# Optimization experiments

Measured on AMD Instinct MI355X. Metric: run time of the kernel, lower is better.

The kernel has to match this reference:

```python
import jax, jax.numpy as jnp
import numpy as np

EMBED_DIM = 512
NUM_HEADS = 8
HEAD_DIM = EMBED_DIM // NUM_HEADS


def setup_inputs() -> dict:
    key = jax.random.key(0)
    ks = jax.random.split(key, 9)
    d = EMBED_DIM
    s = 1.0 / np.sqrt(d)
    inp = {
        "x": jax.random.normal(ks[0], (2, 4096, d), dtype=jnp.float32),
        # torch nn.Linear weights are [out, in]; we store them the same way
        "Wq": jax.random.uniform(ks[1], (d, d), jnp.float32, -s, s),
        "bq": jax.random.uniform(ks[2], (d,), jnp.float32, -s, s),
        "Wk": jax.random.uniform(ks[3], (d, d), jnp.float32, -s, s),
        "bk": jax.random.uniform(ks[4], (d,), jnp.float32, -s, s),
        "Wv": jax.random.uniform(ks[5], (d, d), jnp.float32, -s, s),
        "bv": jax.random.uniform(ks[6], (d,), jnp.float32, -s, s),
        "Wo": jax.random.uniform(ks[7], (d, d), jnp.float32, -s, s),
        "bo": jax.random.uniform(ks[8], (d,), jnp.float32, -s, s),
    }
    return inp


def reference(x, Wq, bq, Wk, bk, Wv, bv, Wo, bo):
    B, S, D = x.shape
    H, Hd = NUM_HEADS, HEAD_DIM

    def proj(W, b):  # torch Linear: x @ W.T + b
        y = jnp.einsum("bsd,ed->bse", x, W) + b
        return y.reshape(B, S, H, Hd).transpose(0, 2, 1, 3)  # [B,H,S,Hd]

    Q = proj(Wq, bq)
    K = proj(Wk, bk)
    V = proj(Wv, bv)

    scale = 1.0 / jnp.sqrt(jnp.float32(Hd))
    scores = jnp.einsum("bhqd,bhkd->bhqk", Q, K) * scale  # [B,H,S,S]
    attn = jax.nn.softmax(scores, axis=-1)
    out = jnp.einsum("bhqk,bhkd->bhqd", attn, V)  # [B,H,S,Hd]
    out = out.transpose(0, 2, 1, 3).reshape(B, S, D)
    return jnp.einsum("bsd,ed->bse", out, Wo) + bo
```

## Files before the change

### kernel.cpp

```cpp
#include <hip/hip_runtime.h>


typedef unsigned short ushortT;
typedef __attribute__((ext_vector_type(8))) short short8;
typedef __attribute__((ext_vector_type(4))) float f32x4;
typedef __attribute__((ext_vector_type(16))) float f32x16;
typedef __attribute__((ext_vector_type(4))) unsigned int uint4v;
typedef __attribute__((ext_vector_type(2))) unsigned int uint2v;

__device__ __forceinline__ ushortT f2bf(float f) {
    unsigned int u = __builtin_bit_cast(unsigned int, f);
    u += 0x7FFFu + ((u >> 16) & 1u);
    return (ushortT)(u >> 16);
}

__device__ __forceinline__ unsigned int cvtpk(float lo, float hi) {
    unsigned int d;
    asm("v_cvt_pk_bf16_f32 %0, %1, %2" : "=v"(d) : "v"(lo), "v"(hi));
    return d;
}

__device__ __forceinline__ uint4v pk8(f32x4 a0, f32x4 a1) {
    uint4v r = { cvtpk(a0[0], a0[1]), cvtpk(a0[2], a0[3]),
                 cvtpk(a1[0], a1[1]), cvtpk(a1[2], a1[3]) };
    return r;
}

__device__ __forceinline__ uint4v ldpk8(const float* p) {
    f32x4 a0 = *(const f32x4*)p;
    f32x4 a1 = *(const f32x4*)(p + 4);
    return pk8(a0, a1);
}

__device__ __forceinline__ void plswap(unsigned int &a, unsigned int &b) {
    uint2v r = __builtin_amdgcn_permlane32_swap(a, b, false, false);
    a = r[0]; b = r[1];
}

#define GLDB 72
#define ALDK 72

__global__ __launch_bounds__(512, 4) void proj_qkv(
    const float* __restrict__ x,
    const float* __restrict__ Wq, const float* __restrict__ bq,
    const float* __restrict__ Wk, const float* __restrict__ bk,
    const float* __restrict__ Wv, const float* __restrict__ bv,
    ushortT* __restrict__ Qw, ushortT* __restrict__ Kw,
    ushortT* __restrict__ Vtw, float qscale)
{
    __shared__ __align__(16) ushortT As[128 * GLDB];
    __shared__ __align__(16) ushortT Bs[128 * GLDB];
    const int t = threadIdx.x;
    const int w = t >> 6, lane = t & 63;
    const int quad = lane >> 4, l15 = lane & 15;
    const int z = blockIdx.z;
    const int bx = blockIdx.x, by = blockIdx.y;
    const int wm = (w >> 1) * 32, wn = (w & 1) * 64;

    const float* W    = (z == 0) ? Wq : (z == 1) ? Wk : Wv;
    const float* bias = (z == 0) ? bq : (z == 1) ? bk : bv;
    const float* Asrc = (z < 2) ? x : W;
    const float* Bsrc = (z < 2) ? W : x;
    const int arow0 = (z < 2) ? bx * 128 : by * 128;
    const int brow0 = (z < 2) ? by * 128 : bx * 128;

    const int sr0 = t >> 3, sc0 = (t & 7) * 8;

    uint4v pka[2], pkb[2];
    pka[0] = ldpk8(Asrc + (size_t)(arow0 + sr0) * 512 + sc0);
    pka[1] = ldpk8(Asrc + (size_t)(arow0 + sr0 + 64) * 512 + sc0);
    pkb[0] = ldpk8(Bsrc + (size_t)(brow0 + sr0) * 512 + sc0);
    pkb[1] = ldpk8(Bsrc + (size_t)(brow0 + sr0 + 64) * 512 + sc0);

    f32x4 acc[2][4] = {};

    for (int k0 = 0; k0 < 512; k0 += 64) {
        *(uint4v*)(As + sr0 * GLDB + sc0) = pka[0];
        *(uint4v*)(As + (sr0 + 64) * GLDB + sc0) = pka[1];
        *(uint4v*)(Bs + sr0 * GLDB + sc0) = pkb[0];
        *(uint4v*)(Bs + (sr0 + 64) * GLDB + sc0) = pkb[1];
        __syncthreads();

        if (k0 < 448) {
            const int kn = k0 + 64;
            pka[0] = ldpk8(Asrc + (size_t)(arow0 + sr0) * 512 + kn + sc0);
            pka[1] = ldpk8(Asrc + (size_t)(arow0 + sr0 + 64) * 512 + kn + sc0);
            pkb[0] = ldpk8(Bsrc + (size_t)(brow0 + sr0) * 512 + kn + sc0);
            pkb[1] = ldpk8(Bsrc + (size_t)(brow0 + sr0 + 64) * 512 + kn + sc0);
        }

#pragma unroll
        for (int kk = 0; kk < 2; kk++) {
            short8 af[2], bfr[4];
#pragma unroll
            for (int i = 0; i < 2; i++)
                af[i] = *(const short8*)(As + (wm + i * 16 + l15) * GLDB + kk * 32 + quad * 8);
#pragma unroll
            for (int i = 0; i < 4; i++)
                bfr[i] = *(const short8*)(Bs + (wn + i * 16 + l15) * GLDB + kk * 32 + quad * 8);
#pragma unroll
            for (int mi = 0; mi < 2; mi++)
#pragma unroll
                for (int ni = 0; ni < 4; ni++)
                    acc[mi][ni] = __builtin_amdgcn_mfma_f32_16x16x32_bf16(
                        af[mi], bfr[ni], acc[mi][ni], 0, 0, 0);
        }
        __syncthreads();
    }

    if (z < 2) {
        ushortT* Y = (z == 0) ? Qw : Kw;
        const float sc = (z == 0) ? qscale : 1.0f;
#pragma unroll
        for (int ni = 0; ni < 4; ni++) {
            int col = brow0 + wn + ni * 16 + l15;
            float bv_ = bias[col];
#pragma unroll
            for (int mi = 0; mi < 2; mi++)
#pragma unroll
                for (int r = 0; r < 4; r++) {
                    int row = arow0 + wm + mi * 16 + quad * 4 + r;
                    Y[(size_t)row * 512 + col] = f2bf((acc[mi][ni][r] + bv_) * sc);
                }
        }
    } else {
        const int bidx = brow0 >> 12;
        const int s0 = brow0 & 4095;
#pragma unroll
        for (int mi = 0; mi < 2; mi++)
#pragma unroll
            for (int r = 0; r < 4; r++) {
                int ch = arow0 + wm + mi * 16 + quad * 4 + r;
                float bv_ = bias[ch];
#pragma unroll
                for (int ni = 0; ni < 4; ni++) {
                    int s = s0 + wn + ni * 16 + l15;
                    Vtw[(size_t)bidx * 2097152 + (size_t)ch * 4096 + s] =
                        f2bf(acc[mi][ni][r] + bv_);
                }
            }
    }
}

__global__ __launch_bounds__(512, 4) void gemm_out(
    const ushortT* __restrict__ X, const float* __restrict__ W,
    const float* __restrict__ bias, float* __restrict__ Y)
{
    __shared__ __align__(16) ushortT As[128 * GLDB];
    __shared__ __align__(16) ushortT Bs[128 * GLDB];
    const int t = threadIdx.x;
    const int w = t >> 6, lane = t & 63;
    const int quad = lane >> 4, l15 = lane & 15;
    const int bm = blockIdx.x * 128, bn = blockIdx.y * 128;
    const int wm = (w >> 1) * 32, wn = (w & 1) * 64;

    const int sr0 = t >> 3, sc0 = (t & 7) * 8;

    uint4v pa[2], pkb[2];
    pa[0] = *(const uint4v*)(X + (size_t)(bm + sr0) * 512 + sc0);
    pa[1] = *(const uint4v*)(X + (size_t)(bm + sr0 + 64) * 512 + sc0);
    pkb[0] = ldpk8(W + (size_t)(bn + sr0) * 512 + sc0);
    pkb[1] = ldpk8(W + (size_t)(bn + sr0 + 64) * 512 + sc0);

    f32x4 acc[2][4] = {};

    for (int k0 = 0; k0 < 512; k0 += 64) {
        *(uint4v*)(As + sr0 * GLDB + sc0) = pa[0];
        *(uint4v*)(As + (sr0 + 64) * GLDB + sc0) = pa[1];
        *(uint4v*)(Bs + sr0 * GLDB + sc0) = pkb[0];
        *(uint4v*)(Bs + (sr0 + 64) * GLDB + sc0) = pkb[1];
        __syncthreads();

        if (k0 < 448) {
            const int kn = k0 + 64;
            pa[0] = *(const uint4v*)(X + (size_t)(bm + sr0) * 512 + kn + sc0);
            pa[1] = *(const uint4v*)(X + (size_t)(bm + sr0 + 64) * 512 + kn + sc0);
            pkb[0] = ldpk8(W + (size_t)(bn + sr0) * 512 + kn + sc0);
            pkb[1] = ldpk8(W + (size_t)(bn + sr0 + 64) * 512 + kn + sc0);
        }

#pragma unroll
        for (int kk = 0; kk < 2; kk++) {
            short8 af[2], bfr[4];
#pragma unroll
            for (int i = 0; i < 2; i++)
                af[i] = *(const short8*)(As + (wm + i * 16 + l15) * GLDB + kk * 32 + quad * 8);
#pragma unroll
            for (int i = 0; i < 4; i++)
                bfr[i] = *(const short8*)(Bs + (wn + i * 16 + l15) * GLDB + kk * 32 + quad * 8);
#pragma unroll
            for (int mi = 0; mi < 2; mi++)
#pragma unroll
                for (int ni = 0; ni < 4; ni++)
                    acc[mi][ni] = __builtin_amdgcn_mfma_f32_16x16x32_bf16(
                        af[mi], bfr[ni], acc[mi][ni], 0, 0, 0);
        }
        __syncthreads();
    }

#pragma unroll
    for (int ni = 0; ni < 4; ni++) {
        int col = bn + wn + ni * 16 + l15;
        float bv = bias[col];
#pragma unroll
        for (int mi = 0; mi < 2; mi++)
#pragma unroll
            for (int r = 0; r < 4; r++) {
                int row = bm + wm + mi * 16 + quad * 4 + r;
                Y[(size_t)row * 512 + col] = acc[mi][ni][r] + bv;
            }
    }
}

__device__ __forceinline__ void softmax_pack(const f32x16 &sacc, float &lp,
                                             uint4v &B0, uint4v &B1)
{
    float p[16];
#pragma unroll
    for (int r = 0; r < 16; r++) {
        p[r] = __builtin_amdgcn_exp2f(sacc[r]);
        lp += p[r];
    }
    unsigned int c00 = cvtpk(p[0],  p[1]),  c01 = cvtpk(p[2],  p[3]);
    unsigned int c10 = cvtpk(p[4],  p[5]),  c11 = cvtpk(p[6],  p[7]);
    unsigned int c20 = cvtpk(p[8],  p[9]),  c21 = cvtpk(p[10], p[11]);
    unsigned int c30 = cvtpk(p[12], p[13]), c31 = cvtpk(p[14], p[15]);
    plswap(c00, c10);
    plswap(c01, c11);
    plswap(c20, c30);
    plswap(c21, c31);
    B0 = uint4v{ c00, c01, c10, c11 };
    B1 = uint4v{ c20, c21, c30, c31 };
}

__global__ __launch_bounds__(512, 2) void attn(
    const ushortT* Q, const ushortT* __restrict__ K,
    const ushortT* __restrict__ Vt, ushortT* O)
{
    __shared__ __align__(16) ushortT SM[2][2][2][64 * ALDK];

    const int t = threadIdx.x;
    const int w = t >> 6, lane = t & 63;
    const int half = w >> 2, qw = w & 3;
    const int l31 = lane & 31, hh = lane >> 5;
    const int qt = blockIdx.x, bh = blockIdx.y;
    const int b = bh >> 3, h = bh & 7;
    const size_t qbase = (size_t)b * 4096 + qt * 256 + qw * 64;

    short8 qf[2][4];
#pragma unroll
    for (int qg = 0; qg < 2; qg++) {
        const ushortT* qp = Q + (qbase + qg * 32 + l31) * 512 + h * 64 + hh * 8;
#pragma unroll
        for (int dk = 0; dk < 4; dk++)
            qf[qg][dk] = *(const short8*)(qp + dk * 16);
    }

    f32x16 oacc[2][2] = {};
    float lpart[2] = {};

    const int kofs = half * 2048;
    const ushortT* Kbase = K + ((size_t)b * 4096 + kofs) * 512 + h * 64;
    const ushortT* Vbase = Vt + (size_t)b * 2097152 + (size_t)h * 64 * 4096 + kofs;

    const int th = t & 255;
    const int srow = th >> 3, scol = (th & 7) * 8;
    uint4v kg[2], vg[2];

#pragma unroll
    for (int i = 0; i < 2; i++) {
        kg[i] = *(const uint4v*)(Kbase + (size_t)(srow + 32 * i) * 512 + scol);
        vg[i] = *(const uint4v*)(Vbase + (size_t)(srow + 32 * i) * 4096 + scol);
    }
#pragma unroll
    for (int i = 0; i < 2; i++) {
        *(uint4v*)(SM[0][half][0] + (srow + 32 * i) * ALDK + scol) = kg[i];
        *(uint4v*)(SM[1][half][0] + (srow + 32 * i) * ALDK + scol) = vg[i];
    }
    __syncthreads();

    for (int kt = 0; kt < 32; kt++) {
        const int cur = kt & 1;

        if (kt < 31) {
            const int kb = (kt + 1) * 64;
#pragma unroll
            for (int i = 0; i < 2; i++) {
                kg[i] = *(const uint4v*)(Kbase + (size_t)(kb + srow + 32 * i) * 512 + scol);
                vg[i] = *(const uint4v*)(Vbase + (size_t)(srow + 32 * i) * 4096 + kb + scol);
            }
        }

        const ushortT* Kt  = SM[0][half][cur];
        const ushortT* Vtl = SM[1][half][cur];

#pragma unroll
        for (int st = 0; st < 2; st++) {
            short8 kf[4];
#pragma unroll
            for (int dk = 0; dk < 4; dk++)
                kf[dk] = *(const short8*)(Kt + (st * 32 + l31) * ALDK + dk * 16 + hh * 8);
            f32x16 s0 = {}, s1 = {};
#pragma unroll
            for (int dk = 0; dk < 4; dk++) {
                s0 = __builtin_amdgcn_mfma_f32_32x32x16_bf16(kf[dk], qf[0][dk], s0, 0, 0, 0);
                s1 = __builtin_amdgcn_mfma_f32_32x32x16_bf16(kf[dk], qf[1][dk], s1, 0, 0, 0);
            }

            uint4v B00, B01, B10, B11;
            softmax_pack(s0, lpart[0], B00, B01);
            softmax_pack(s1, lpart[1], B10, B11);
            short8 p00 = __builtin_bit_cast(short8, B00);
            short8 p01 = __builtin_bit_cast(short8, B01);
            short8 p10 = __builtin_bit_cast(short8, B10);
            short8 p11 = __builtin_bit_cast(short8, B11);

#pragma unroll
            for (int dt = 0; dt < 2; dt++) {
                short8 vf0 = *(const short8*)(Vtl + (dt * 32 + l31) * ALDK + st * 32 + hh * 8);
                short8 vf1 = *(const short8*)(Vtl + (dt * 32 + l31) * ALDK + st * 32 + 16 + hh * 8);
                oacc[0][dt] = __builtin_amdgcn_mfma_f32_32x32x16_bf16(vf0, p00, oacc[0][dt], 0, 0, 0);
                oacc[0][dt] = __builtin_amdgcn_mfma_f32_32x32x16_bf16(vf1, p01, oacc[0][dt], 0, 0, 0);
                oacc[1][dt] = __builtin_amdgcn_mfma_f32_32x32x16_bf16(vf0, p10, oacc[1][dt], 0, 0, 0);
                oacc[1][dt] = __builtin_amdgcn_mfma_f32_32x32x16_bf16(vf1, p11, oacc[1][dt], 0, 0, 0);
            }
        }

        if (kt < 31) {
            const int nb = cur ^ 1;
#pragma unroll
            for (int i = 0; i < 2; i++) {
                *(uint4v*)(SM[0][half][nb] + (srow + 32 * i) * ALDK + scol) = kg[i];
                *(uint4v*)(SM[1][half][nb] + (srow + 32 * i) * ALDK + scol) = vg[i];
            }
        }
        __syncthreads();
    }

    float* scratch = (float*)&SM[0][0][0][0];
    float* prow = scratch + (size_t)(qw * 64 + lane) * 68;

    if (half == 1) {
#pragma unroll
        for (int qg = 0; qg < 2; qg++)
#pragma unroll
            for (int dt = 0; dt < 2; dt++)
#pragma unroll
                for (int m = 0; m < 4; m++) {
                    f32x4 v4 = { oacc[qg][dt][4 * m + 0], oacc[qg][dt][4 * m + 1],
                                 oacc[qg][dt][4 * m + 2], oacc[qg][dt][4 * m + 3] };
                    *(f32x4*)(prow + qg * 32 + dt * 16 + m * 4) = v4;
                }
        prow[64] = lpart[0];
        prow[65] = lpart[1];
    }
    __syncthreads();

    if (half == 0) {
#pragma unroll
        for (int qg = 0; qg < 2; qg++) {
            float sum = lpart[qg] + prow[64 + qg];
            float l = sum + __shfl_xor(sum, 32);
            float rl = 1.0f / l;

            ushortT* orow = O + (qbase + qg * 32 + l31) * 512 + h * 64 + hh * 4;
#pragma unroll
            for (int dt = 0; dt < 2; dt++)
#pragma unroll
                for (int m = 0; m < 4; m++) {
                    f32x4 v4 = *(const f32x4*)(prow + qg * 32 + dt * 16 + m * 4);
                    unsigned int u0 = cvtpk((oacc[qg][dt][4 * m + 0] + v4[0]) * rl,
                                            (oacc[qg][dt][4 * m + 1] + v4[1]) * rl);
                    unsigned int u1 = cvtpk((oacc[qg][dt][4 * m + 2] + v4[2]) * rl,
                                            (oacc[qg][dt][4 * m + 3] + v4[3]) * rl);
                    uint2v st2 = { u0, u1 };
                    *(uint2v*)(orow + dt * 32 + m * 8) = st2;
                }
        }
    }
}

extern "C" void kernel_launch(void* const* d_in, const int* in_sizes, int n_in,
                              void* d_out, int out_size, void* d_ws, size_t ws_size,
                              hipStream_t stream)
{
    const float* x  = (const float*)d_in[0];
    const float* Wq = (const float*)d_in[1];
    const float* bq = (const float*)d_in[2];
    const float* Wk = (const float*)d_in[3];
    const float* bk = (const float*)d_in[4];
    const float* Wv = (const float*)d_in[5];
    const float* bv = (const float*)d_in[6];
    const float* Wo = (const float*)d_in[7];
    const float* bo = (const float*)d_in[8];

    ushortT* ws  = (ushortT*)d_ws;
    ushortT* Qw  = ws;
    ushortT* Kw  = ws + 4194304;
    ushortT* Vtw = ws + 2 * 4194304;

    const float qscale = 0.125f * 1.44269504089f;

    proj_qkv<<<dim3(64, 4, 3), 512, 0, stream>>>(
        x, Wq, bq, Wk, bk, Wv, bv, Qw, Kw, Vtw, qscale);
    attn<<<dim3(16, 16), 512, 0, stream>>>(Qw, Kw, Vtw, Qw);
    gemm_out<<<dim3(64, 4), 512, 0, stream>>>(Qw, Wo, bo, (float*)d_out);
}
```

Baseline: 196.6 us.

## Fuse Q/K/V projections into one block sharing the x tile

The QKV projection kernel now computes all three projections in one block. Each x tile is loaded and converted to bf16 once and reused against three weight tiles, where before three separate z-slices each reloaded it. The V output is now computed as x·Wv^T instead of Wv·x^T, with a transposed store using packed 2-element bf16 writes. The grid shrinks to a third and each block holds three accumulator sets and three B tiles in LDS. That raises register and LDS pressure, so the launch bound drops to 2 blocks per CU.

```diff
diff --git a/kernel.cpp b/kernel.cpp
--- a/kernel.cpp
+++ b/kernel.cpp
@@ -40,7 +40,7 @@
 #define GLDB 72
 #define ALDK 72
 
-__global__ __launch_bounds__(512, 4) void proj_qkv(
+__global__ __launch_bounds__(512, 2) void proj_qkv(
     const float* __restrict__ x,
     const float* __restrict__ Wq, const float* __restrict__ bq,
     const float* __restrict__ Wk, const float* __restrict__ bk,
@@ -49,67 +49,77 @@
     ushortT* __restrict__ Vtw, float qscale)
 {
     __shared__ __align__(16) ushortT As[128 * GLDB];
-    __shared__ __align__(16) ushortT Bs[128 * GLDB];
+    __shared__ __align__(16) ushortT Bs[3][128 * GLDB];
     const int t = threadIdx.x;
     const int w = t >> 6, lane = t & 63;
     const int quad = lane >> 4, l15 = lane & 15;
-    const int z = blockIdx.z;
-    const int bx = blockIdx.x, by = blockIdx.y;
+    const int arow0 = blockIdx.x * 128;
+    const int brow0 = blockIdx.y * 128;
     const int wm = (w >> 1) * 32, wn = (w & 1) * 64;
 
-    const float* W    = (z == 0) ? Wq : (z == 1) ? Wk : Wv;
-    const float* bias = (z == 0) ? bq : (z == 1) ? bk : bv;
-    const float* Asrc = (z < 2) ? x : W;
-    const float* Bsrc = (z < 2) ? W : x;
-    const int arow0 = (z < 2) ? bx * 128 : by * 128;
-    const int brow0 = (z < 2) ? by * 128 : bx * 128;
+    const float* Wsrc[3] = { Wq, Wk, Wv };
 
     const int sr0 = t >> 3, sc0 = (t & 7) * 8;
 
-    uint4v pka[2], pkb[2];
-    pka[0] = ldpk8(Asrc + (size_t)(arow0 + sr0) * 512 + sc0);
-    pka[1] = ldpk8(Asrc + (size_t)(arow0 + sr0 + 64) * 512 + sc0);
-    pkb[0] = ldpk8(Bsrc + (size_t)(brow0 + sr0) * 512 + sc0);
-    pkb[1] = ldpk8(Bsrc + (size_t)(brow0 + sr0 + 64) * 512 + sc0);
-
-    f32x4 acc[2][4] = {};
+    uint4v pka[2], pkb[3][2];
+    pka[0] = ldpk8(x + (size_t)(arow0 + sr0) * 512 + sc0);
+    pka[1] = ldpk8(x + (size_t)(arow0 + sr0 + 64) * 512 + sc0);
+#pragma unroll
+    for (int z = 0; z < 3; z++) {
+        pkb[z][0] = ldpk8(Wsrc[z] + (size_t)(brow0 + sr0) * 512 + sc0);
+        pkb[z][1] = ldpk8(Wsrc[z] + (size_t)(brow0 + sr0 + 64) * 512 + sc0);
+    }
+
+    f32x4 acc[3][2][4] = {};
 
     for (int k0 = 0; k0 < 512; k0 += 64) {
         *(uint4v*)(As + sr0 * GLDB + sc0) = pka[0];
         *(uint4v*)(As + (sr0 + 64) * GLDB + sc0) = pka[1];
-        *(uint4v*)(Bs + sr0 * GLDB + sc0) = pkb[0];
-        *(uint4v*)(Bs + (sr0 + 64) * GLDB + sc0) = pkb[1];
+#pragma unroll
+        for (int z = 0; z < 3; z++) {
+            *(uint4v*)(Bs[z] + sr0 * GLDB + sc0) = pkb[z][0];
+            *(uint4v*)(Bs[z] + (sr0 + 64) * GLDB + sc0) = pkb[z][1];
+        }
         __syncthreads();
 
         if (k0 < 448) {
             const int kn = k0 + 64;
-            pka[0] = ldpk8(Asrc + (size_t)(arow0 + sr0) * 512 + kn + sc0);
-            pka[1] = ldpk8(Asrc + (size_t)(arow0 + sr0 + 64) * 512 + kn + sc0);
-            pkb[0] = ldpk8(Bsrc + (size_t)(brow0 + sr0) * 512 + kn + sc0);
-            pkb[1] = ldpk8(Bsrc + (size_t)(brow0 + sr0 + 64) * 512 + kn + sc0);
+            pka[0] = ldpk8(x + (size_t)(arow0 + sr0) * 512 + kn + sc0);
+            pka[1] = ldpk8(x + (size_t)(arow0 + sr0 + 64) * 512 + kn + sc0);
+#pragma unroll
+            for (int z = 0; z < 3; z++) {
+                pkb[z][0] = ldpk8(Wsrc[z] + (size_t)(brow0 + sr0) * 512 + kn + sc0);
+                pkb[z][1] = ldpk8(Wsrc[z] + (size_t)(brow0 + sr0 + 64) * 512 + kn + sc0);
+            }
         }
 
 #pragma unroll
         for (int kk = 0; kk < 2; kk++) {
-            short8 af[2], bfr[4];
+            short8 af[2];
 #pragma unroll
             for (int i = 0; i < 2; i++)
                 af[i] = *(const short8*)(As + (wm + i * 16 + l15) * GLDB + kk * 32 + quad * 8);
 #pragma unroll
-            for (int i = 0; i < 4; i++)
-                bfr[i] = *(const short8*)(Bs + (wn + i * 16 + l15) * GLDB + kk * 32 + quad * 8);
-#pragma unroll
-            for (int mi = 0; mi < 2; mi++)
-#pragma unroll
-                for (int ni = 0; ni < 4; ni++)
-                    acc[mi][ni] = __builtin_amdgcn_mfma_f32_16x16x32_bf16(
-                        af[mi], bfr[ni], acc[mi][ni], 0, 0, 0);
+            for (int z = 0; z < 3; z++) {
+                short8 bfr[4];
+#pragma unroll
+                for (int i = 0; i < 4; i++)
+                    bfr[i] = *(const short8*)(Bs[z] + (wn + i * 16 + l15) * GLDB + kk * 32 + quad * 8);
+#pragma unroll
+                for (int mi = 0; mi < 2; mi++)
+#pragma unroll
+                    for (int ni = 0; ni < 4; ni++)
+                        acc[z][mi][ni] = __builtin_amdgcn_mfma_f32_16x16x32_bf16(
+                            af[mi], bfr[ni], acc[z][mi][ni], 0, 0, 0);
+            }
         }
         __syncthreads();
     }
 
-    if (z < 2) {
+#pragma unroll
+    for (int z = 0; z < 2; z++) {
         ushortT* Y = (z == 0) ? Qw : Kw;
+        const float* bias = (z == 0) ? bq : bk;
         const float sc = (z == 0) ? qscale : 1.0f;
 #pragma unroll
         for (int ni = 0; ni < 4; ni++) {
@@ -120,25 +130,28 @@
 #pragma unroll
                 for (int r = 0; r < 4; r++) {
                     int row = arow0 + wm + mi * 16 + quad * 4 + r;
-                    Y[(size_t)row * 512 + col] = f2bf((acc[mi][ni][r] + bv_) * sc);
+                    Y[(size_t)row * 512 + col] = f2bf((acc[z][mi][ni][r] + bv_) * sc);
                 }
         }
-    } else {
-        const int bidx = brow0 >> 12;
-        const int s0 = brow0 & 4095;
-#pragma unroll
-        for (int mi = 0; mi < 2; mi++)
-#pragma unroll
-            for (int r = 0; r < 4; r++) {
-                int ch = arow0 + wm + mi * 16 + quad * 4 + r;
-                float bv_ = bias[ch];
-#pragma unroll
-                for (int ni = 0; ni < 4; ni++) {
-                    int s = s0 + wn + ni * 16 + l15;
-                    Vtw[(size_t)bidx * 2097152 + (size_t)ch * 4096 + s] =
-                        f2bf(acc[mi][ni][r] + bv_);
-                }
-            }
+    }
+
+    {
+        const int bidx = arow0 >> 12;
+        const int s0 = (arow0 & 4095) + wm;
+#pragma unroll
+        for (int ni = 0; ni < 4; ni++) {
+            int ch = brow0 + wn + ni * 16 + l15;
+            float bv_ = bv[ch];
+            ushortT* vrow = Vtw + (size_t)bidx * 2097152 + (size_t)ch * 4096;
+#pragma unroll
+            for (int mi = 0; mi < 2; mi++) {
+                int s = s0 + mi * 16 + quad * 4;
+                unsigned int u0 = cvtpk(acc[2][mi][ni][0] + bv_, acc[2][mi][ni][1] + bv_);
+                unsigned int u1 = cvtpk(acc[2][mi][ni][2] + bv_, acc[2][mi][ni][3] + bv_);
+                uint2v st2 = { u0, u1 };
+                *(uint2v*)(vrow + s) = st2;
+            }
+        }
     }
 }
 
@@ -401,7 +414,7 @@
 
     const float qscale = 0.125f * 1.44269504089f;
 
-    proj_qkv<<<dim3(64, 4, 3), 512, 0, stream>>>(
+    proj_qkv<<<dim3(64, 4), 512, 0, stream>>>(
         x, Wq, bq, Wk, bk, Wv, bv, Qw, Kw, Vtw, qscale);
     attn<<<dim3(16, 16), 512, 0, stream>>>(Qw, Kw, Vtw, Qw);
     gemm_out<<<dim3(64, 4), 512, 0, stream>>>(Qw, Wo, bo, (float*)d_out);
```

New measurement: 199.1 us. No clear change (+1.3%).
